# Optimization experiments

Measured on AMD Instinct MI355X. Metric: run time of the kernel, lower is better.

The kernel has to match this reference:

```python
import jax, jax.numpy as jnp
import numpy as np

B, C, H, IN = 128, 1024, 256, 19  # batch, subcarriers, hidden, input dim
P = 2 * H                          # prism input dim (att + rad features)
NL = 8                             # layers in attenuation/radiance nets
UEBS = 2 * 4                       # num_ue_antennas * num_bs_antennas


def _init(key, shape, scale=0.02):
    return (jax.random.normal(key, shape, dtype=jnp.float32) * scale)


def setup_inputs() -> dict:
    key = jax.random.key(0)
    ks = jax.random.split(key, 24)
    return {
        "positions": jax.random.normal(ks[0], (B, 3), dtype=jnp.float32),
        "ue_antennas": jax.random.normal(ks[1], (B, 2), dtype=jnp.float32),
        "bs_antennas": jax.random.normal(ks[2], (B, 4), dtype=jnp.float32),
        "additional_features": jax.random.normal(ks[3], (B, 10), dtype=jnp.float32),
        "att_W1": _init(ks[4], (IN, H)), "att_b1": _init(ks[5], (H,)),
        "att_Wh": _init(ks[6], (NL - 1, H, H)), "att_bh": _init(ks[7], (NL - 1, H)),
        # radiance net: same structure
        "rad_W1": _init(ks[8], (IN, H)), "rad_b1": _init(ks[9], (H,)),
        "rad_Wh": _init(ks[10], (NL - 1, H, H)), "rad_bh": _init(ks[11], (NL - 1, H)),
        # RF prism: per-subcarrier stacked weights
        "prism_W1": _init(ks[12], (C, P, H)), "prism_b1": _init(ks[13], (C, H)),
        "prism_W2": _init(ks[14], (C, H, H)), "prism_b2": _init(ks[15], (C, H)),
        "prism_W3": _init(ks[16], (C, H)), "prism_b3": _init(ks[17], (C,)),
        # mimo head: Linear(1 -> ue*bs)
        "mimo_W": _init(ks[18], (1, UEBS)), "mimo_b": _init(ks[19], (UEBS,)),
    }


def _deep_mlp(x, W1, b1, Wh, bh):
    h = jax.nn.relu(x @ W1 + b1)
    def step(h, wb):
        W, b = wb
        return jax.nn.relu(h @ W + b), None
    h, _ = jax.lax.scan(step, h, (Wh, bh))
    return h


def reference(positions, ue_antennas, bs_antennas, additional_features,
              att_W1, att_b1, att_Wh, att_bh,
              rad_W1, rad_b1, rad_Wh, rad_bh,
              prism_W1, prism_b1, prism_W2, prism_b2, prism_W3, prism_b3,
              mimo_W, mimo_b):
    x = jnp.concatenate([positions, ue_antennas, bs_antennas, additional_features], axis=1)  # [B,19]
    att = _deep_mlp(x, att_W1, att_b1, att_Wh, att_bh)  # [B,H]
    rad = _deep_mlp(x, rad_W1, rad_b1, rad_Wh, rad_bh)  # [B,H]
    feat = jnp.concatenate([att, rad], axis=1)  # [B,2H]
    # batched per-subcarrier 3-layer MLPs (grouped GEMMs)
    h1 = jax.nn.relu(jnp.einsum('bi,cio->bco', feat, prism_W1) + prism_b1)  # [B,C,H]
    h2 = jax.nn.relu(jnp.einsum('bch,cho->bco', h1, prism_W2) + prism_b2)   # [B,C,H]
    sub = jnp.einsum('bch,ch->bc', h2, prism_W3) + prism_b3                 # [B,C]
    mimo = sub.mean(axis=1, keepdims=True) @ mimo_W + mimo_b                # [B,8]
    return sub, mimo
```

## Files before the change

kernel.cpp:

```cpp
#include <hip/hip_runtime.h>
#include <hip/hip_bf16.h>
#include <stdint.h>

#define Bv 128
#define Hv 256
#define INv 19
#define Pv 512
#define Cv 1024
#define NLh 7

typedef __attribute__((ext_vector_type(4))) float floatx4;
typedef __attribute__((ext_vector_type(8))) short shortx8;
typedef __attribute__((ext_vector_type(4))) unsigned int uintx4;

__device__ __forceinline__ unsigned short f2bf(float f) {
    union { float f; unsigned int u; } v; v.f = f;
    unsigned int r = v.u + 0x7fffu + ((v.u >> 16) & 1u);
    return (unsigned short)(r >> 16);
}

__device__ __forceinline__ int swz(int r) { return ((r & 7) ^ ((r >> 3) & 7)); }

#define BAR() do { asm volatile("s_waitcnt lgkmcnt(0)" ::: "memory"); \
                   __builtin_amdgcn_s_barrier(); } while (0)

__global__ __launch_bounds__(256) void mlp_fused(
    const float* __restrict__ pos, const float* __restrict__ ue,
    const float* __restrict__ bs,  const float* __restrict__ addf,
    const float* __restrict__ attW1, const float* __restrict__ attb1,
    const float* __restrict__ attWh, const float* __restrict__ attbh,
    const float* __restrict__ radW1, const float* __restrict__ radb1,
    const float* __restrict__ radWh, const float* __restrict__ radbh,
    unsigned short* __restrict__ feat)
{
    int blk = blockIdx.x;
    int net = blk >> 6, bq = blk & 63;
    const float* W1 = net ? radW1 : attW1;
    const float* b1 = net ? radb1 : attb1;
    const float* Wh = net ? radWh : attWh;
    const float* bh = net ? radbh : attbh;
    __shared__ float xs[2][INv];
    __shared__ float hr[2][Hv];
    __shared__ float part[4][2][Hv];
    int t = threadIdx.x;
    if (t < 2 * INv) {
        int r = t / INv, k = t - r * INv;
        int b = bq * 2 + r;
        float v;
        if (k < 3) v = pos[b*3 + k];
        else if (k < 5) v = ue[b*2 + (k-3)];
        else if (k < 9) v = bs[b*4 + (k-5)];
        else v = addf[b*10 + (k-9)];
        xs[r][k] = v;
    }
    __syncthreads();
    {
        float a0 = b1[t], a1 = a0;
        #pragma unroll
        for (int k = 0; k < INv; ++k) {
            float w = W1[k*Hv + t];
            a0 += xs[0][k] * w;
            a1 += xs[1][k] * w;
        }
        hr[0][t] = fmaxf(a0, 0.f);
        hr[1][t] = fmaxf(a1, 0.f);
    }
    __syncthreads();
    int half = t >> 6, oq = t & 63;
    for (int layer = 0; layer < NLh; ++layer) {
        const float* W = Wh + (size_t)layer * Hv * Hv;
        const float* Wp = W + (size_t)(half * 64) * Hv + oq * 4;
        floatx4 a0r0 = {0.f,0.f,0.f,0.f}, a1r0 = {0.f,0.f,0.f,0.f};
        floatx4 a0r1 = {0.f,0.f,0.f,0.f}, a1r1 = {0.f,0.f,0.f,0.f};
        #pragma unroll 8
        for (int kk = 0; kk < 64; kk += 2) {
            floatx4 w0 = *reinterpret_cast<const floatx4*>(Wp + (size_t)kk * Hv);
            floatx4 w1 = *reinterpret_cast<const floatx4*>(Wp + (size_t)(kk+1) * Hv);
            float h00 = hr[0][half*64 + kk], h01 = hr[0][half*64 + kk + 1];
            float h10 = hr[1][half*64 + kk], h11 = hr[1][half*64 + kk + 1];
            a0r0 += w0 * h00; a1r0 += w1 * h01;
            a0r1 += w0 * h10; a1r1 += w1 * h11;
        }
        floatx4 r0 = a0r0 + a1r0, r1 = a0r1 + a1r1;
        *reinterpret_cast<floatx4*>(&part[half][0][oq*4]) = r0;
        *reinterpret_cast<floatx4*>(&part[half][1][oq*4]) = r1;
        __syncthreads();
        int r = t >> 7, o2 = (t & 127) * 2;
        const float* bias = bh + layer * Hv;
        float s0 = part[0][r][o2]   + part[1][r][o2]   + part[2][r][o2]   + part[3][r][o2]   + bias[o2];
        float s1 = part[0][r][o2+1] + part[1][r][o2+1] + part[2][r][o2+1] + part[3][r][o2+1] + bias[o2+1];
        s0 = fmaxf(s0, 0.f); s1 = fmaxf(s1, 0.f);
        if (layer == NLh - 1) {
            feat[(size_t)(bq*2 + r) * Pv + net*Hv + o2]     = f2bf(s0);
            feat[(size_t)(bq*2 + r) * Pv + net*Hv + o2 + 1] = f2bf(s1);
        } else {
            hr[r][o2] = s0; hr[r][o2+1] = s1;
        }
        __syncthreads();
    }
}


__device__ __forceinline__ void stage_w(const float* __restrict__ Wc, int t,
                                        int kg, int oq, floatx4* r) {
    const float* s = Wc + (size_t)(t*64 + kg*8) * 256 + oq*4;
    #pragma unroll
    for (int i = 0; i < 8; ++i) r[i] = *reinterpret_cast<const floatx4*>(s + i*256);
}

__device__ __forceinline__ void write_w(char* wb, int kg, int oq, const floatx4* r) {
    #pragma unroll
    for (int j = 0; j < 4; ++j) {
        int o = oq*4 + j;
        unsigned int p0 = (unsigned int)f2bf(r[0][j]) | ((unsigned int)f2bf(r[1][j]) << 16);
        unsigned int p1 = (unsigned int)f2bf(r[2][j]) | ((unsigned int)f2bf(r[3][j]) << 16);
        unsigned int p2 = (unsigned int)f2bf(r[4][j]) | ((unsigned int)f2bf(r[5][j]) << 16);
        unsigned int p3 = (unsigned int)f2bf(r[6][j]) | ((unsigned int)f2bf(r[7][j]) << 16);
        uintx4 v = {p0, p1, p2, p3};
        int slot = kg ^ swz(o);
        *reinterpret_cast<uintx4*>(wb + o*128 + slot*16) = v;
    }
}

__device__ __forceinline__ void stage_a(const unsigned short* __restrict__ feat,
                                        int t, int tid, uintx4* r) {
    #pragma unroll
    for (int q = 0; q < 2; ++q) {
        int si = tid + q*512, row = si >> 3, s = si & 7;
        r[q] = *reinterpret_cast<const uintx4*>(feat + row*Pv + t*64 + s*8);
    }
}

__device__ __forceinline__ void write_a(char* ab, int tid, const uintx4* r) {
    #pragma unroll
    for (int q = 0; q < 2; ++q) {
        int si = tid + q*512, row = si >> 3, s = si & 7;
        int slot = s ^ swz(row);
        *reinterpret_cast<uintx4*>(ab + row*128 + slot*16) = r[q];
    }
}

__device__ __forceinline__ void mfma_chunk_l1(const char* ab, const char* wb,
                                              int wm, int wn, int l,
                                              floatx4 (&acc)[4][4]) {
    #pragma unroll
    for (int ks = 0; ks < 2; ++ks) {
        shortx8 af[4], bf[4];
        #pragma unroll
        for (int m = 0; m < 4; ++m) {
            int row = wm*64 + m*16 + (l & 15);
            int slot = (ks*4 + (l >> 4)) ^ swz(row);
            af[m] = *reinterpret_cast<const shortx8*>(ab + row*128 + slot*16);
        }
        #pragma unroll
        for (int n = 0; n < 4; ++n) {
            int o = wn*64 + n*16 + (l & 15);
            int slot = (ks*4 + (l >> 4)) ^ swz(o);
            bf[n] = *reinterpret_cast<const shortx8*>(wb + o*128 + slot*16);
        }
        #pragma unroll
        for (int m = 0; m < 4; ++m)
            #pragma unroll
            for (int n = 0; n < 4; ++n)
                acc[m][n] = __builtin_amdgcn_mfma_f32_16x16x32_bf16(af[m], bf[n], acc[m][n], 0, 0, 0);
    }
}

__device__ __forceinline__ void mfma_chunk_l2(const char* h1, const char* wb, int t2,
                                              int wm, int wn, int l,
                                              floatx4 (&acc)[4][4]) {
    #pragma unroll
    for (int ks = 0; ks < 2; ++ks) {
        shortx8 af[4], bf[4];
        #pragma unroll
        for (int m = 0; m < 4; ++m) {
            int row = wm*64 + m*16 + (l & 15);
            int k2 = t2*64 + ks*32 + (l >> 4)*8;
            af[m] = *reinterpret_cast<const shortx8*>(h1 + row*512 + ((k2*2) ^ (swz(row) << 4)));
        }
        #pragma unroll
        for (int n = 0; n < 4; ++n) {
            int o = wn*64 + n*16 + (l & 15);
            int slot = (ks*4 + (l >> 4)) ^ swz(o);
            bf[n] = *reinterpret_cast<const shortx8*>(wb + o*128 + slot*16);
        }
        #pragma unroll
        for (int m = 0; m < 4; ++m)
            #pragma unroll
            for (int n = 0; n < 4; ++n)
                acc[m][n] = __builtin_amdgcn_mfma_f32_16x16x32_bf16(af[m], bf[n], acc[m][n], 0, 0, 0);
    }
}


__global__ __launch_bounds__(512) void prism_kernel(
    const unsigned short* __restrict__ feat,
    const float* __restrict__ W1, const float* __restrict__ b1,
    const float* __restrict__ W2, const float* __restrict__ b2,
    const float* __restrict__ W3, const float* __restrict__ b3,
    float* __restrict__ out)
{
    __shared__ __align__(16) char smem[131072];
    const int c = blockIdx.x;
    const int tid = threadIdx.x;
    const int l = tid & 63;
    const int w = tid >> 6;
    const int wm = w >> 2;
    const int wn = w & 3;
    const int kg = w;
    const int oq = l;

    const float* W1c = W1 + (size_t)c * (Pv * Hv);
    const float* W2c = W2 + (size_t)c * (Hv * Hv);

    char* ab0 = smem;
    char* ab1 = smem + 16384;
    char* wb0 = smem + 32768;
    char* wb1 = smem + 65536;
    char* h1  = smem;
    char* w2b0 = smem + 65536;
    char* w2b1 = smem + 98304;
    float* subws = (float*)smem;

    float bias1v[4], bias2v[4], w3v[4];
    #pragma unroll
    for (int n = 0; n < 4; ++n) {
        int o = wn*64 + n*16 + (l & 15);
        bias1v[n] = b1[c*Hv + o];
        bias2v[n] = b2[c*Hv + o];
        w3v[n]    = W3[c*Hv + o];
    }
    float b3v = b3[c];

    floatx4 wr0[8], wr1[8];
    uintx4 ar0[2], ar1[2];

    stage_w(W1c, 0, kg, oq, wr0);
    stage_a(feat, 0, tid, ar0);
    stage_w(W1c, 1, kg, oq, wr1);
    stage_a(feat, 1, tid, ar1);
    write_w(wb0, kg, oq, wr0);
    write_a(ab0, tid, ar0);
    BAR();

    floatx4 acc[4][4];
    #pragma unroll
    for (int m = 0; m < 4; ++m)
        #pragma unroll
        for (int n = 0; n < 4; ++n)
            acc[m][n] = (floatx4){0.f, 0.f, 0.f, 0.f};

    #pragma unroll
    for (int t = 0; t < 8; ++t) {
        if (t + 2 < 8) {
            if ((t & 1) == 0) { stage_w(W1c, t+2, kg, oq, wr0); stage_a(feat, t+2, tid, ar0); }
            else              { stage_w(W1c, t+2, kg, oq, wr1); stage_a(feat, t+2, tid, ar1); }
        } else if (t == 6) {
            stage_w(W2c, 0, kg, oq, wr0);
        } else {
            stage_w(W2c, 1, kg, oq, wr1);
        }
        const char* ab = (t & 1) ? ab1 : ab0;
        const char* wb = (t & 1) ? wb1 : wb0;
        mfma_chunk_l1(ab, wb, wm, wn, l, acc);
        if (t + 1 < 8) {
            char* abn = ((t+1) & 1) ? ab1 : ab0;
            char* wbn = ((t+1) & 1) ? wb1 : wb0;
            if ((t+1) & 1) { write_w(wbn, kg, oq, wr1); write_a(abn, tid, ar1); }
            else           { write_w(wbn, kg, oq, wr0); write_a(abn, tid, ar0); }
        }
        BAR();
    }

    #pragma unroll
    for (int m = 0; m < 4; ++m) {
        #pragma unroll
        for (int n = 0; n < 4; ++n) {
            int o = wn*64 + n*16 + (l & 15);
            #pragma unroll
            for (int jj = 0; jj < 4; ++jj) {
                int bb = wm*64 + m*16 + (l >> 4)*4 + jj;
                float v = fmaxf(acc[m][n][jj] + bias1v[n], 0.f);
                *(unsigned short*)(h1 + bb*512 + ((o*2) ^ (swz(bb) << 4))) = f2bf(v);
            }
        }
    }
    write_w(w2b0, kg, oq, wr0);
    BAR();

    floatx4 acc2[4][4];
    #pragma unroll
    for (int m = 0; m < 4; ++m)
        #pragma unroll
        for (int n = 0; n < 4; ++n)
            acc2[m][n] = (floatx4){0.f, 0.f, 0.f, 0.f};

    #pragma unroll
    for (int t = 0; t < 4; ++t) {
        if (t + 2 < 4) {
            if ((t & 1) == 0) stage_w(W2c, t+2, kg, oq, wr0);
            else              stage_w(W2c, t+2, kg, oq, wr1);
        }
        const char* wb = (t & 1) ? w2b1 : w2b0;
        mfma_chunk_l2(h1, wb, t, wm, wn, l, acc2);
        if (t + 1 < 4) {
            char* wbn = ((t+1) & 1) ? w2b1 : w2b0;
            if ((t+1) & 1) write_w(wbn, kg, oq, wr1);
            else           write_w(wbn, kg, oq, wr0);
        }
        BAR();
    }

    float p[4][4];
    #pragma unroll
    for (int m = 0; m < 4; ++m)
        #pragma unroll
        for (int jj = 0; jj < 4; ++jj) {
            float s = 0.f;
            #pragma unroll
            for (int n = 0; n < 4; ++n)
                s += fmaxf(acc2[m][n][jj] + bias2v[n], 0.f) * w3v[n];
            p[m][jj] = s;
        }
    #pragma unroll
    for (int m = 0; m < 4; ++m)
        #pragma unroll
        for (int jj = 0; jj < 4; ++jj) {
            p[m][jj] += __shfl_xor(p[m][jj], 1, 64);
            p[m][jj] += __shfl_xor(p[m][jj], 2, 64);
            p[m][jj] += __shfl_xor(p[m][jj], 4, 64);
            p[m][jj] += __shfl_xor(p[m][jj], 8, 64);
        }
    BAR();
    {
        int t16 = l & 15;
        float pv = 0.f;
        #pragma unroll
        for (int m = 0; m < 4; ++m)
            #pragma unroll
            for (int jj = 0; jj < 4; ++jj)
                if (m == (t16 >> 2) && jj == (t16 & 3)) pv = p[m][jj];
        int bb = wm*64 + (t16 >> 2)*16 + (l >> 4)*4 + (t16 & 3);
        subws[wn*128 + bb] = pv;
    }
    BAR();
    if (tid < 128) {
        float s = subws[tid] + subws[128 + tid] + subws[256 + tid] + subws[384 + tid] + b3v;
        out[(size_t)tid * Cv + c] = s;
    }
}


__global__ __launch_bounds__(256) void mimo_kernel(
    const float* __restrict__ sub, const float* __restrict__ mW,
    const float* __restrict__ mB, float* __restrict__ out)
{
    int b = blockIdx.x;
    int t = threadIdx.x;
    float s = 0.f;
    #pragma unroll
    for (int j = 0; j < 4; ++j) s += sub[b*Cv + t + j*256];
    #pragma unroll
    for (int m = 1; m < 64; m <<= 1) s += __shfl_xor(s, m, 64);
    __shared__ float red[4];
    if ((t & 63) == 0) red[t >> 6] = s;
    __syncthreads();
    if (t < 8) {
        float mean = (red[0] + red[1] + red[2] + red[3]) * (1.0f / 1024.0f);
        out[Bv * Cv + b*8 + t] = mean * mW[t] + mB[t];
    }
}


extern "C" void kernel_launch(void* const* d_in, const int* in_sizes, int n_in,
                              void* d_out, int out_size, void* d_ws, size_t ws_size,
                              hipStream_t stream) {
    (void)in_sizes; (void)n_in; (void)out_size; (void)ws_size;
    const float* pos   = (const float*)d_in[0];
    const float* ue    = (const float*)d_in[1];
    const float* bsant = (const float*)d_in[2];
    const float* addf  = (const float*)d_in[3];
    const float* attW1 = (const float*)d_in[4];
    const float* attb1 = (const float*)d_in[5];
    const float* attWh = (const float*)d_in[6];
    const float* attbh = (const float*)d_in[7];
    const float* radW1 = (const float*)d_in[8];
    const float* radb1 = (const float*)d_in[9];
    const float* radWh = (const float*)d_in[10];
    const float* radbh = (const float*)d_in[11];
    const float* pW1   = (const float*)d_in[12];
    const float* pb1   = (const float*)d_in[13];
    const float* pW2   = (const float*)d_in[14];
    const float* pb2   = (const float*)d_in[15];
    const float* pW3   = (const float*)d_in[16];
    const float* pb3   = (const float*)d_in[17];
    const float* mW    = (const float*)d_in[18];
    const float* mB    = (const float*)d_in[19];
    float* out = (float*)d_out;

    unsigned short* feat = (unsigned short*)d_ws;

    mlp_fused<<<128, 256, 0, stream>>>(pos, ue, bsant, addf,
                                       attW1, attb1, attWh, attbh,
                                       radW1, radb1, radWh, radbh, feat);
    prism_kernel<<<Cv, 512, 0, stream>>>(feat, pW1, pb1, pW2, pb2, pW3, pb3, out);
    mimo_kernel<<<Bv, 256, 0, stream>>>(out, mW, mB, out);
}
```

Baseline: 202.8 us.

## Process four subcarriers per block with cross-subcarrier weight prefetch, direct global A loads

Each prism block now handles four consecutive subcarriers in a loop, prefetching the next subcarrier's first W1 tiles during the current layer-2 loop so weight streaming continues across subcarrier boundaries. Layer-1 activation fragments are read straight from global memory (feat is small and cache-resident) instead of being staged through LDS, and LDS is re-partitioned into two weight buffers, an h1 buffer and a reduction area. The grid shrinks from 1024 to 256 blocks, which on a large-CU GPU may leave compute units underused and lengthen the tail, and global A loads add latency inside the MFMA loop.

Result: slower. 446.8 us (+120.3%).

```diff
diff --git a/kernel.cpp b/kernel.cpp
--- a/kernel.cpp
+++ b/kernel.cpp
@@ -101,11 +101,11 @@
 }
 
 
-__device__ __forceinline__ void stage_w(const float* __restrict__ Wc, int t,
-                                        int kg, int oq, floatx4* r) {
-    const float* s = Wc + (size_t)(t*64 + kg*8) * 256 + oq*4;
-    #pragma unroll
-    for (int i = 0; i < 8; ++i) r[i] = *reinterpret_cast<const floatx4*>(s + i*256);
+__device__ __forceinline__ void stage_w_p(const float* __restrict__ src,
+                                          int kg, int oq, floatx4* r) {
+    const float* p = src + (size_t)(kg * 8) * Hv + oq * 4;
+    #pragma unroll
+    for (int i = 0; i < 8; ++i) r[i] = *reinterpret_cast<const floatx4*>(p + i * Hv);
 }
 
 __device__ __forceinline__ void write_w(char* wb, int kg, int oq, const floatx4* r) {
@@ -122,35 +122,18 @@
     }
 }
 
-__device__ __forceinline__ void stage_a(const unsigned short* __restrict__ feat,
-                                        int t, int tid, uintx4* r) {
-    #pragma unroll
-    for (int q = 0; q < 2; ++q) {
-        int si = tid + q*512, row = si >> 3, s = si & 7;
-        r[q] = *reinterpret_cast<const uintx4*>(feat + row*Pv + t*64 + s*8);
-    }
-}
-
-__device__ __forceinline__ void write_a(char* ab, int tid, const uintx4* r) {
-    #pragma unroll
-    for (int q = 0; q < 2; ++q) {
-        int si = tid + q*512, row = si >> 3, s = si & 7;
-        int slot = s ^ swz(row);
-        *reinterpret_cast<uintx4*>(ab + row*128 + slot*16) = r[q];
-    }
-}
-
-__device__ __forceinline__ void mfma_chunk_l1(const char* ab, const char* wb,
-                                              int wm, int wn, int l,
-                                              floatx4 (&acc)[4][4]) {
+__device__ __forceinline__ void mfma_l1g(const unsigned short* __restrict__ feat,
+                                         int t, const char* wb,
+                                         int wm, int wn, int l,
+                                         floatx4 (&acc)[4][4]) {
     #pragma unroll
     for (int ks = 0; ks < 2; ++ks) {
         shortx8 af[4], bf[4];
         #pragma unroll
         for (int m = 0; m < 4; ++m) {
             int row = wm*64 + m*16 + (l & 15);
-            int slot = (ks*4 + (l >> 4)) ^ swz(row);
-            af[m] = *reinterpret_cast<const shortx8*>(ab + row*128 + slot*16);
+            af[m] = *reinterpret_cast<const shortx8*>(
+                feat + (size_t)row * Pv + t*64 + ks*32 + (l >> 4)*8);
         }
         #pragma unroll
         for (int n = 0; n < 4; ++n) {
@@ -166,9 +149,9 @@
     }
 }
 
-__device__ __forceinline__ void mfma_chunk_l2(const char* h1, const char* wb, int t2,
-                                              int wm, int wn, int l,
-                                              floatx4 (&acc)[4][4]) {
+__device__ __forceinline__ void mfma_l2(const char* h1, const char* wb, int t2,
+                                        int wm, int wn, int l,
+                                        floatx4 (&acc)[4][4]) {
     #pragma unroll
     for (int ks = 0; ks < 2; ++ks) {
         shortx8 af[4], bf[4];
@@ -193,15 +176,18 @@
 }
 
 
-__global__ __launch_bounds__(512) void prism_kernel(
+__global__ __launch_bounds__(512, 2) void prism_kernel(
     const unsigned short* __restrict__ feat,
     const float* __restrict__ W1, const float* __restrict__ b1,
     const float* __restrict__ W2, const float* __restrict__ b2,
     const float* __restrict__ W3, const float* __restrict__ b3,
     float* __restrict__ out)
 {
-    __shared__ __align__(16) char smem[131072];
-    const int c = blockIdx.x;
+    __shared__ __align__(16) char smem[133120];
+    char* bufs[2] = { smem, smem + 32768 };
+    char* h1 = smem + 65536;
+    float* subws = (float*)(smem + 131072);
+
     const int tid = threadIdx.x;
     const int l = tid & 63;
     const int w = tid >> 6;
@@ -210,143 +196,119 @@
     const int kg = w;
     const int oq = l;
 
-    const float* W1c = W1 + (size_t)c * (Pv * Hv);
-    const float* W2c = W2 + (size_t)c * (Hv * Hv);
-
-    char* ab0 = smem;
-    char* ab1 = smem + 16384;
-    char* wb0 = smem + 32768;
-    char* wb1 = smem + 65536;
-    char* h1  = smem;
-    char* w2b0 = smem + 65536;
-    char* w2b1 = smem + 98304;
-    float* subws = (float*)smem;
-
-    float bias1v[4], bias2v[4], w3v[4];
-    #pragma unroll
-    for (int n = 0; n < 4; ++n) {
-        int o = wn*64 + n*16 + (l & 15);
-        bias1v[n] = b1[c*Hv + o];
-        bias2v[n] = b2[c*Hv + o];
-        w3v[n]    = W3[c*Hv + o];
-    }
-    float b3v = b3[c];
-
-    floatx4 wr0[8], wr1[8];
-    uintx4 ar0[2], ar1[2];
-
-    stage_w(W1c, 0, kg, oq, wr0);
-    stage_a(feat, 0, tid, ar0);
-    stage_w(W1c, 1, kg, oq, wr1);
-    stage_a(feat, 1, tid, ar1);
-    write_w(wb0, kg, oq, wr0);
-    write_a(ab0, tid, ar0);
+    const int c0 = blockIdx.x * 4;
+
+    floatx4 wr[2][8];
+
+    stage_w_p(W1 + (size_t)c0 * (Pv*Hv), kg, oq, wr[0]);
+    stage_w_p(W1 + (size_t)c0 * (Pv*Hv) + (size_t)64 * Hv, kg, oq, wr[1]);
+    write_w(bufs[0], kg, oq, wr[0]);
     BAR();
 
-    floatx4 acc[4][4];
-    #pragma unroll
-    for (int m = 0; m < 4; ++m)
-        #pragma unroll
-        for (int n = 0; n < 4; ++n)
-            acc[m][n] = (floatx4){0.f, 0.f, 0.f, 0.f};
-
-    #pragma unroll
-    for (int t = 0; t < 8; ++t) {
-        if (t + 2 < 8) {
-            if ((t & 1) == 0) { stage_w(W1c, t+2, kg, oq, wr0); stage_a(feat, t+2, tid, ar0); }
-            else              { stage_w(W1c, t+2, kg, oq, wr1); stage_a(feat, t+2, tid, ar1); }
-        } else if (t == 6) {
-            stage_w(W2c, 0, kg, oq, wr0);
-        } else {
-            stage_w(W2c, 1, kg, oq, wr1);
-        }
-        const char* ab = (t & 1) ? ab1 : ab0;
-        const char* wb = (t & 1) ? wb1 : wb0;
-        mfma_chunk_l1(ab, wb, wm, wn, l, acc);
-        if (t + 1 < 8) {
-            char* abn = ((t+1) & 1) ? ab1 : ab0;
-            char* wbn = ((t+1) & 1) ? wb1 : wb0;
-            if ((t+1) & 1) { write_w(wbn, kg, oq, wr1); write_a(abn, tid, ar1); }
-            else           { write_w(wbn, kg, oq, wr0); write_a(abn, tid, ar0); }
-        }
-        BAR();
-    }
-
-    #pragma unroll
-    for (int m = 0; m < 4; ++m) {
+    for (int k = 0; k < 4; ++k) {
+        const int c = c0 + k;
+        const float* W1c = W1 + (size_t)c * (Pv * Hv);
+        const float* W2c = W2 + (size_t)c * (Hv * Hv);
+        const float* W1n = W1 + (size_t)(c + 1) * (Pv * Hv);
+
+        float bias1v[4], bias2v[4], w3v[4];
         #pragma unroll
         for (int n = 0; n < 4; ++n) {
             int o = wn*64 + n*16 + (l & 15);
+            bias1v[n] = b1[c*Hv + o];
+            bias2v[n] = b2[c*Hv + o];
+            w3v[n]    = W3[c*Hv + o];
+        }
+        float b3v = b3[c];
+
+        floatx4 acc[4][4];
+        #pragma unroll
+        for (int m = 0; m < 4; ++m)
+            #pragma unroll
+            for (int n = 0; n < 4; ++n)
+                acc[m][n] = (floatx4){0.f, 0.f, 0.f, 0.f};
+
+        #pragma unroll
+        for (int t = 0; t < 8; ++t) {
+            const float* ps = (t < 6) ? W1c + (size_t)(t + 2) * 64 * Hv
+                                      : W2c + (size_t)(t - 6) * 64 * Hv;
+            stage_w_p(ps, kg, oq, wr[t & 1]);
+            mfma_l1g(feat, t, bufs[t & 1], wm, wn, l, acc);
+            write_w(bufs[(t + 1) & 1], kg, oq, wr[(t + 1) & 1]);
+            BAR();
+        }
+
+        #pragma unroll
+        for (int m = 0; m < 4; ++m) {
+            #pragma unroll
+            for (int n = 0; n < 4; ++n) {
+                int o = wn*64 + n*16 + (l & 15);
+                #pragma unroll
+                for (int jj = 0; jj < 4; ++jj) {
+                    int bb = wm*64 + m*16 + (l >> 4)*4 + jj;
+                    float v = fmaxf(acc[m][n][jj] + bias1v[n], 0.f);
+                    *(unsigned short*)(h1 + bb*512 + ((o*2) ^ (swz(bb) << 4))) = f2bf(v);
+                }
+            }
+        }
+        BAR();
+
+        #pragma unroll
+        for (int m = 0; m < 4; ++m)
+            #pragma unroll
+            for (int n = 0; n < 4; ++n)
+                acc[m][n] = (floatx4){0.f, 0.f, 0.f, 0.f};
+
+        #pragma unroll
+        for (int t = 0; t < 4; ++t) {
+            if (t < 2) {
+                stage_w_p(W2c + (size_t)(t + 2) * 64 * Hv, kg, oq, wr[t & 1]);
+            } else if (k < 3) {
+                stage_w_p(W1n + (size_t)(t - 2) * 64 * Hv, kg, oq, wr[t & 1]);
+            }
+            mfma_l2(h1, bufs[t & 1], t, wm, wn, l, acc);
+            if (!(k == 3 && t == 3))
+                write_w(bufs[(t + 1) & 1], kg, oq, wr[(t + 1) & 1]);
+            BAR();
+        }
+
+        float p[4][4];
+        #pragma unroll
+        for (int m = 0; m < 4; ++m)
             #pragma unroll
             for (int jj = 0; jj < 4; ++jj) {
-                int bb = wm*64 + m*16 + (l >> 4)*4 + jj;
-                float v = fmaxf(acc[m][n][jj] + bias1v[n], 0.f);
-                *(unsigned short*)(h1 + bb*512 + ((o*2) ^ (swz(bb) << 4))) = f2bf(v);
+                float s = 0.f;
+                #pragma unroll
+                for (int n = 0; n < 4; ++n)
+                    s += fmaxf(acc[m][n][jj] + bias2v[n], 0.f) * w3v[n];
+                p[m][jj] = s;
             }
-        }
-    }
-    write_w(w2b0, kg, oq, wr0);
-    BAR();
-
-    floatx4 acc2[4][4];
-    #pragma unroll
-    for (int m = 0; m < 4; ++m)
-        #pragma unroll
-        for (int n = 0; n < 4; ++n)
-            acc2[m][n] = (floatx4){0.f, 0.f, 0.f, 0.f};
-
-    #pragma unroll
-    for (int t = 0; t < 4; ++t) {
-        if (t + 2 < 4) {
-            if ((t & 1) == 0) stage_w(W2c, t+2, kg, oq, wr0);
-            else              stage_w(W2c, t+2, kg, oq, wr1);
-        }
-        const char* wb = (t & 1) ? w2b1 : w2b0;
-        mfma_chunk_l2(h1, wb, t, wm, wn, l, acc2);
-        if (t + 1 < 4) {
-            char* wbn = ((t+1) & 1) ? w2b1 : w2b0;
-            if ((t+1) & 1) write_w(wbn, kg, oq, wr1);
-            else           write_w(wbn, kg, oq, wr0);
+        #pragma unroll
+        for (int m = 0; m < 4; ++m)
+            #pragma unroll
+            for (int jj = 0; jj < 4; ++jj) {
+                p[m][jj] += __shfl_xor(p[m][jj], 1, 64);
+                p[m][jj] += __shfl_xor(p[m][jj], 2, 64);
+                p[m][jj] += __shfl_xor(p[m][jj], 4, 64);
+                p[m][jj] += __shfl_xor(p[m][jj], 8, 64);
+            }
+        {
+            int t16 = l & 15;
+            float pv = 0.f;
+            #pragma unroll
+            for (int m = 0; m < 4; ++m)
+                #pragma unroll
+                for (int jj = 0; jj < 4; ++jj)
+                    if (m == (t16 >> 2) && jj == (t16 & 3)) pv = p[m][jj];
+            int bb = wm*64 + (t16 >> 2)*16 + (l >> 4)*4 + (t16 & 3);
+            subws[wn*128 + bb] = pv;
         }
         BAR();
-    }
-
-    float p[4][4];
-    #pragma unroll
-    for (int m = 0; m < 4; ++m)
-        #pragma unroll
-        for (int jj = 0; jj < 4; ++jj) {
-            float s = 0.f;
-            #pragma unroll
-            for (int n = 0; n < 4; ++n)
-                s += fmaxf(acc2[m][n][jj] + bias2v[n], 0.f) * w3v[n];
-            p[m][jj] = s;
-        }
-    #pragma unroll
-    for (int m = 0; m < 4; ++m)
-        #pragma unroll
-        for (int jj = 0; jj < 4; ++jj) {
-            p[m][jj] += __shfl_xor(p[m][jj], 1, 64);
-            p[m][jj] += __shfl_xor(p[m][jj], 2, 64);
-            p[m][jj] += __shfl_xor(p[m][jj], 4, 64);
-            p[m][jj] += __shfl_xor(p[m][jj], 8, 64);
-        }
-    BAR();
-    {
-        int t16 = l & 15;
-        float pv = 0.f;
-        #pragma unroll
-        for (int m = 0; m < 4; ++m)
-            #pragma unroll
-            for (int jj = 0; jj < 4; ++jj)
-                if (m == (t16 >> 2) && jj == (t16 & 3)) pv = p[m][jj];
-        int bb = wm*64 + (t16 >> 2)*16 + (l >> 4)*4 + (t16 & 3);
-        subws[wn*128 + bb] = pv;
-    }
-    BAR();
-    if (tid < 128) {
-        float s = subws[tid] + subws[128 + tid] + subws[256 + tid] + subws[384 + tid] + b3v;
-        out[(size_t)tid * Cv + c] = s;
+        if (tid < 128) {
+            float s = subws[tid] + subws[128 + tid] + subws[256 + tid] + subws[384 + tid] + b3v;
+            out[(size_t)tid * Cv + c] = s;
+        }
+        BAR();
     }
 }
 
@@ -403,6 +365,6 @@
     mlp_fused<<<128, 256, 0, stream>>>(pos, ue, bsant, addf,
                                        attW1, attb1, attWh, attbh,
                                        radW1, radb1, radWh, radbh, feat);
-    prism_kernel<<<Cv, 512, 0, stream>>>(feat, pW1, pb1, pW2, pb2, pW3, pb3, out);
+    prism_kernel<<<Cv / 4, 512, 0, stream>>>(feat, pW1, pb1, pW2, pb2, pW3, pb3, out);
     mimo_kernel<<<Bv, 256, 0, stream>>>(out, mW, mB, out);
 }
```
